# Optimization experiments

Measured on AMD Instinct MI355X. Metric: run time of the kernel, lower is better.

The kernel has to match this reference:

```python
import jax, jax.numpy as jnp
import numpy as np

N_NODES = 40000
N_EDGES = 640000
D = 128
BN_EPS = 1e-5
GATE_EPS = 1e-6


def _linear_params(key, d_in, d_out):
    kw, kb = jax.random.split(key)
    bound = 1.0 / np.sqrt(d_in)
    W = jax.random.uniform(kw, (d_out, d_in), jnp.float32, -bound, bound)
    b = jax.random.uniform(kb, (d_out,), jnp.float32, -bound, bound)
    return W, b


def setup_inputs() -> dict:
    key = jax.random.key(0)
    ks = jax.random.split(key, 8)
    x = jax.random.normal(ks[0], (N_NODES, D), jnp.float32)
    edge_index = jax.random.randint(ks[1], (2, N_EDGES), 0, N_NODES, jnp.int64)
    edge_attr = jax.random.normal(ks[2], (N_EDGES, D), jnp.float32)
    W_src_gate, b_src_gate = _linear_params(ks[3], D, D)
    W_dst_gate, b_dst_gate = _linear_params(ks[4], D, D)
    W_edge_gate, b_edge_gate = _linear_params(ks[5], D, D)
    W_src_update, b_src_update = _linear_params(ks[6], D, D)
    W_dst_update, b_dst_update = _linear_params(ks[7], D, D)
    return dict(
        x=x, edge_index=edge_index, edge_attr=edge_attr,
        W_src_gate=W_src_gate, b_src_gate=b_src_gate,
        W_dst_gate=W_dst_gate, b_dst_gate=b_dst_gate,
        W_edge_gate=W_edge_gate, b_edge_gate=b_edge_gate,
        W_src_update=W_src_update, b_src_update=b_src_update,
        W_dst_update=W_dst_update, b_dst_update=b_dst_update,
        bn_nodes_gamma=jnp.ones((D,), jnp.float32), bn_nodes_beta=jnp.zeros((D,), jnp.float32),
        bn_edges_gamma=jnp.ones((D,), jnp.float32), bn_edges_beta=jnp.zeros((D,), jnp.float32),
    )


def _batch_norm(z, gamma, beta):
    # training-mode BN: batch mean, biased variance (torch semantics)
    mean = jnp.mean(z, axis=0)
    var = jnp.mean(jnp.square(z - mean), axis=0)
    return gamma * (z - mean) * jax.lax.rsqrt(var + BN_EPS) + beta


def reference(x, edge_index, edge_attr,
              W_src_gate, b_src_gate, W_dst_gate, b_dst_gate,
              W_edge_gate, b_edge_gate, W_src_update, b_src_update,
              W_dst_update, b_dst_update,
              bn_nodes_gamma, bn_nodes_beta, bn_edges_gamma, bn_edges_beta):
    row, col = edge_index[0], edge_index[1]
    num_nodes = x.shape[0]
    x_row = x[row]                      # [E, D] gather
    x_col = x[col]                      # [E, D] gather
    e_src = x_row @ W_src_gate.T + b_src_gate
    e_dst = x_col @ W_dst_gate.T + b_dst_gate
    m = e_src + e_dst + edge_attr @ W_edge_gate.T + b_edge_gate  # [E, D]
    sigma = jax.nn.sigmoid(m)
    h_weighted = (x_col @ W_dst_update.T + b_dst_update) * sigma
    h_sum = jax.ops.segment_sum(h_weighted, col, num_segments=num_nodes)
    sigma_sum = jax.ops.segment_sum(sigma, col, num_segments=num_nodes)
    h_normalized = h_sum / (sigma_sum + GATE_EPS)
    x_new = x @ W_src_update.T + b_src_update + h_normalized
    x_new = jax.nn.softplus(_batch_norm(x_new, bn_nodes_gamma, bn_nodes_beta))
    y_new = jax.nn.softplus(_batch_norm(m, bn_edges_gamma, bn_edges_beta))
    x_new = x + x_new          # residual
    y_new = edge_attr + y_new  # residual
    return (x_new, y_new)
```

## Files before the change

kernel.cpp:

```cpp
#include <hip/hip_runtime.h>

#define NN 40000
#define NE 640000

typedef unsigned short u16;
typedef unsigned int u32;
typedef __attribute__((ext_vector_type(4))) float f32x4;
typedef __attribute__((ext_vector_type(4))) float fv4;
typedef __attribute__((ext_vector_type(4))) u32 uv4;
typedef __attribute__((ext_vector_type(8))) __bf16 bf16x8;

#define LSTR 132
#define TPW 8

__device__ __forceinline__ float bf2f(u16 u) { return __uint_as_float(((u32)u) << 16); }
__device__ __forceinline__ u16 f2bf(float f) {
  u32 u = __float_as_uint(f);
  u32 r = 0x7fffu + ((u >> 16) & 1u);
  return (u16)((u + r) >> 16);
}
__device__ __forceinline__ float splus(float v) {
  return fmaxf(v, 0.0f) + __logf(1.0f + __expf(-fabsf(v)));
}

__global__ void sniff_k(const u32* __restrict__ gamma, const u32* __restrict__ eidx,
                        u32* __restrict__ flags) {
  if (threadIdx.x == 0) {
    flags[0] = (gamma[0] == 0x3F803F80u) ? 1u : 0u;
    u32 odd = eidx[1] | eidx[3] | eidx[5] | eidx[7] |
              eidx[9] | eidx[11] | eidx[13] | eidx[15];
    flags[1] = (odd == 0u) ? 1u : 0u;
  }
}

__device__ __forceinline__ int load_col(const void* eidx, int e, u32 i64) {
  int nc = i64 ? (int)((const u32*)eidx)[2 * ((size_t)NE + e)]
               : ((const int*)eidx)[NE + e];
  return min(max(nc, 0), NN - 1);
}
__device__ __forceinline__ int load_row(const void* eidx, int e, u32 i64) {
  int nr = i64 ? (int)((const u32*)eidx)[2 * (size_t)e]
               : ((const int*)eidx)[e];
  return min(max(nr, 0), NN - 1);
}

__global__ __launch_bounds__(256) void wconv5_k(
    const float* __restrict__ W0, const float* __restrict__ W1,
    const float* __restrict__ W2, const float* __restrict__ W3,
    const float* __restrict__ W4, u16* __restrict__ out) {
  int i = blockIdx.x * 256 + threadIdx.x;
  int mtx = blockIdx.y;
  const float* W = (mtx == 0) ? W0 : (mtx == 1) ? W1 : (mtx == 2) ? W2
                 : (mtx == 3) ? W3 : W4;
  out[mtx * 16384 + i] = f2bf(W[i]);
}

__global__ __launch_bounds__(256) void hist_k(const void* __restrict__ eidx,
                                              u32* __restrict__ cnt,
                                              const u32* __restrict__ flags) {
  int e = blockIdx.x * 256 + threadIdx.x;
  atomicAdd(&cnt[load_col(eidx, e, flags[1])], 1u);
}

__device__ __forceinline__ bf16x8 a_frag(const float* __restrict__ row, int kbase) {
  float4 f0 = *(const float4*)(row + kbase);
  float4 f1 = *(const float4*)(row + kbase + 4);
  bf16x8 a;
  a[0] = (__bf16)f0.x; a[1] = (__bf16)f0.y; a[2] = (__bf16)f0.z; a[3] = (__bf16)f0.w;
  a[4] = (__bf16)f1.x; a[5] = (__bf16)f1.y; a[6] = (__bf16)f1.z; a[7] = (__bf16)f1.w;
  return a;
}

__device__ __forceinline__ bf16x8 cvt8v(fv4 a, fv4 b) {
  bf16x8 r;
  r[0] = (__bf16)a[0]; r[1] = (__bf16)a[1]; r[2] = (__bf16)a[2]; r[3] = (__bf16)a[3];
  r[4] = (__bf16)b[0]; r[5] = (__bf16)b[1]; r[6] = (__bf16)b[2]; r[7] = (__bf16)b[3];
  return r;
}

__device__ __forceinline__ void gemm16(const bf16x8 af[4], const u16* __restrict__ Wb,
                                       const float* __restrict__ bias, int lane,
                                       f32x4 acc[8]) {
  int l15 = lane & 15, lk = lane >> 4;
#pragma unroll
  for (int n = 0; n < 8; ++n) {
    float bv = bias[n * 16 + l15];
    acc[n] = (f32x4){bv, bv, bv, bv};
  }
#pragma unroll
  for (int n = 0; n < 8; ++n) {
    const u16* bp = Wb + (size_t)(n * 16 + l15) * 128 + lk * 8;
#pragma unroll
    for (int k = 0; k < 4; ++k) {
      bf16x8 b = *(const bf16x8*)(bp + 32 * k);
      acc[n] = __builtin_amdgcn_mfma_f32_16x16x32_bf16(af[k], b, acc[n], 0, 0, 0);
    }
  }
}

__device__ __forceinline__ void store_tile(u16* __restrict__ out, int m0, int lane,
                                           const f32x4 acc[8]) {
  int l15 = lane & 15, lk = lane >> 4;
#pragma unroll
  for (int n = 0; n < 8; ++n)
#pragma unroll
    for (int r = 0; r < 4; ++r)
      out[(size_t)(m0 + lk * 4 + r) * 128 + n * 16 + l15] = f2bf(acc[n][r]);
}

__global__ __launch_bounds__(256) void node_gemm_k(
    const float* __restrict__ x, const u16* __restrict__ Wb,
    const float* __restrict__ B0, const float* __restrict__ B1,
    const float* __restrict__ B2, const float* __restrict__ B3,
    const u32* __restrict__ cnt,
    u16* __restrict__ o0, u16* __restrict__ o1,
    u16* __restrict__ o2, u16* __restrict__ o3,
    float* __restrict__ statsg) {
  __shared__ float red[256];
  int tid = threadIdx.x, lane = tid & 63, w = tid >> 6;
  for (int i = tid; i < 256; i += 256) red[i] = 0.f;
  __syncthreads();
  int m0 = blockIdx.x * 64 + w * 16;
  int l15 = lane & 15, lk = lane >> 4;
  const float* arow = x + (size_t)(m0 + l15) * 128;
  bf16x8 af[4];
#pragma unroll
  for (int k = 0; k < 4; ++k) af[k] = a_frag(arow, 32 * k + 8 * lk);
  f32x4 acc[8], accd[8];
  gemm16(af, Wb + 0 * 16384, B0, lane, acc);  store_tile(o0, m0, lane, acc);
  gemm16(af, Wb + 1 * 16384, B1, lane, acc);  store_tile(o1, m0, lane, acc);
  gemm16(af, Wb + 2 * 16384, B2, lane, accd); store_tile(o2, m0, lane, accd);
  gemm16(af, Wb + 3 * 16384, B3, lane, acc);  store_tile(o3, m0, lane, acc);
  float g[4];
#pragma unroll
  for (int r = 0; r < 4; ++r) g[r] = (cnt[m0 + lk * 4 + r] != 0u) ? 1.0f : 0.0f;
#pragma unroll
  for (int n = 0; n < 8; ++n) {
    float a1 = 0.f, a2 = 0.f;
#pragma unroll
    for (int r = 0; r < 4; ++r) {
      float zv = acc[n][r] + g[r] * accd[n][r];
      a1 += zv;
      a2 = fmaf(zv, zv, a2);
    }
    a1 += __shfl_xor(a1, 16); a1 += __shfl_xor(a1, 32);
    a2 += __shfl_xor(a2, 16); a2 += __shfl_xor(a2, 32);
    if (lk == 0) {
      atomicAdd(&red[n * 16 + l15], a1);
      atomicAdd(&red[128 + n * 16 + l15], a2);
    }
  }
  __syncthreads();
  for (int i = tid; i < 256; i += 256) atomicAdd(&statsg[256 + i], red[i]);
}

__global__ __launch_bounds__(256, 2) void edge_gemm_k(
    const float* __restrict__ ea, const u16* __restrict__ Wgb,
    const float* __restrict__ Bg,
    const u16* __restrict__ g_src, const u16* __restrict__ g_dst,
    const void* __restrict__ eidx,
    u16* __restrict__ mge, float* __restrict__ statsg,
    const u32* __restrict__ flags) {
  __shared__ __align__(16) char gbuf[4][16 * LSTR * 4];
  __shared__ __align__(16) u16 Wl[16384];
  int tid = threadIdx.x, lane = tid & 63, w = tid >> 6;
  int l15 = lane & 15, lk = lane >> 4;
  int el = lane >> 2, c4 = lane & 3;
  u32 i64 = flags[1];

  {
    const u32* Wg32 = (const u32*)Wgb;
    u32* Wl32 = (u32*)Wl;
#pragma unroll
    for (int j = 0; j < 32; ++j) {
      int i2 = tid + 256 * j;
      int r = i2 >> 6, c2 = i2 & 63;
      int g = c2 >> 2, win = c2 & 3;
      Wl32[r * 64 + (((g ^ ((r & 7) << 1)) << 2) | win)] = Wg32[i2];
    }
  }
  __syncthreads();

  float* gt = (float*)gbuf[w];
  u16*   mt = (u16*)gbuf[w];
  int sw = (l15 & 7) << 1;

  float bias[8];
#pragma unroll
  for (int n = 0; n < 8; ++n) bias[n] = Bg[n * 16 + l15];

  float e1[8] = {0.f, 0.f, 0.f, 0.f, 0.f, 0.f, 0.f, 0.f};
  float e2[8] = {0.f, 0.f, 0.f, 0.f, 0.f, 0.f, 0.f, 0.f};

  int base = (blockIdx.x * 4 + w) * (TPW * 16);
  const float* aptr = ea + (size_t)(base + l15) * 128 + 8 * lk;

  fv4 tmp[8];
#pragma unroll
  for (int k = 0; k < 4; ++k) {
    tmp[2 * k]     = *(const fv4*)(aptr + 32 * k);
    tmp[2 * k + 1] = *(const fv4*)(aptr + 32 * k + 4);
  }
  bf16x8 af[4];
#pragma unroll
  for (int k = 0; k < 4; ++k) af[k] = cvt8v(tmp[2 * k], tmp[2 * k + 1]);

  for (int t = 0; t < TPW; ++t) {
    int e0 = base + t * 16;
    int eg = e0 + el;
    int grow = load_row(eidx, eg, i64);
    int gcol = load_col(eidx, eg, i64);
#pragma unroll
    for (int it = 0; it < 4; ++it) {
      uv4 gsv = *(const uv4*)(g_src + (size_t)grow * 128 + c4 * 8 + it * 32);
      uv4 gdv = *(const uv4*)(g_dst + (size_t)gcol * 128 + c4 * 8 + it * 32);
      const u16* sp = (const u16*)&gsv;
      const u16* dp = (const u16*)&gdv;
      fv4 lo, hi;
#pragma unroll
      for (int j = 0; j < 4; ++j) lo[j] = bf2f(sp[j]) + bf2f(dp[j]);
#pragma unroll
      for (int j = 0; j < 4; ++j) hi[j] = bf2f(sp[4 + j]) + bf2f(dp[4 + j]);
      int ch = c4 + 4 * it;
      *(fv4*)(gt + el * LSTR + ch * 8)     = lo;
      *(fv4*)(gt + el * LSTR + ch * 8 + 4) = hi;
    }
    if (t + 1 < TPW) {
      const float* anx = aptr + (size_t)(t + 1) * 16 * 128;
#pragma unroll
      for (int k = 0; k < 4; ++k) {
        tmp[2 * k]     = *(const fv4*)(anx + 32 * k);
        tmp[2 * k + 1] = *(const fv4*)(anx + 32 * k + 4);
      }
    }
    f32x4 acc[8];
#pragma unroll
    for (int n = 0; n < 8; ++n)
      acc[n] = (f32x4){bias[n], bias[n], bias[n], bias[n]};
#pragma unroll
    for (int n = 0; n < 8; ++n)
#pragma unroll
      for (int k = 0; k < 4; ++k) {
        bf16x8 b = *(const bf16x8*)(Wl + ((n * 16 + l15) << 7) +
                                    (((lk + 4 * k) ^ sw) << 3));
        acc[n] = __builtin_amdgcn_mfma_f32_16x16x32_bf16(af[k], b, acc[n], 0, 0, 0);
      }
    float g32[8][4];
#pragma unroll
    for (int n = 0; n < 8; ++n)
#pragma unroll
      for (int r = 0; r < 4; ++r)
        g32[n][r] = gt[(lk * 4 + r) * LSTR + n * 16 + l15];
    __builtin_amdgcn_sched_barrier(0);
#pragma unroll
    for (int n = 0; n < 8; ++n)
#pragma unroll
      for (int r = 0; r < 4; ++r) {
        float mv = acc[n][r] + g32[n][r];
        e1[n] += mv;
        e2[n] = fmaf(mv, mv, e2[n]);
        mt[(lk * 4 + r) * LSTR + n * 16 + l15] = f2bf(mv);
      }
    if (t + 1 < TPW) {
#pragma unroll
      for (int k = 0; k < 4; ++k) af[k] = cvt8v(tmp[2 * k], tmp[2 * k + 1]);
    }
#pragma unroll
    for (int it = 0; it < 4; ++it) {
      int ch = c4 + 4 * it;
      uint4 v = *(const uint4*)(mt + el * LSTR + ch * 8);
      *(uint4*)(mge + (size_t)(e0 + el) * 128 + ch * 8) = v;
    }
  }
#pragma unroll
  for (int n = 0; n < 8; ++n) {
    float s1 = e1[n], s2 = e2[n];
    s1 += __shfl_xor(s1, 16); s1 += __shfl_xor(s1, 32);
    s2 += __shfl_xor(s2, 16); s2 += __shfl_xor(s2, 32);
    if (lk == 0) {
      atomicAdd(&statsg[n * 16 + l15], s1);
      atomicAdd(&statsg[128 + n * 16 + l15], s2);
    }
  }
}

__global__ void stats_fin_k(const float* __restrict__ es1, const float* __restrict__ es2,
                            const float* __restrict__ ns1, const float* __restrict__ ns2,
                            const float* __restrict__ eg_, const float* __restrict__ eb_,
                            const float* __restrict__ ng_, const float* __restrict__ nb_,
                            float* __restrict__ params) {
  int d = threadIdx.x;
  float em = es1[d] * (1.0f / NE);
  float ev = fmaxf(es2[d] * (1.0f / NE) - em * em, 0.0f);
  float esc = eg_[d] * rsqrtf(ev + 1e-5f);
  params[d] = esc;
  params[128 + d] = eb_[d] - em * esc;
  float nm = ns1[d] * (1.0f / NN);
  float nv = fmaxf(ns2[d] * (1.0f / NN) - nm * nm, 0.0f);
  float nsc = ng_[d] * rsqrtf(nv + 1e-5f);
  params[256 + d] = nsc;
  params[384 + d] = nb_[d] - nm * nsc;
}

__global__ __launch_bounds__(256) void node_fin2_k(
    const float* __restrict__ x, const u16* __restrict__ us,
    const u16* __restrict__ ud, const u32* __restrict__ cnt,
    const float* __restrict__ params, float* __restrict__ out) {
  size_t t = (size_t)blockIdx.x * 256 + threadIdx.x;
  size_t base = t * 8;
  int d0 = (int)(base & 127);
  int n = (int)(t >> 4);
  float g = (cnt[n] != 0u) ? 1.0f : 0.0f;
  float4 xa = *(const float4*)(x + base);
  float4 xb = *(const float4*)(x + base + 4);
  float xv[8] = {xa.x, xa.y, xa.z, xa.w, xb.x, xb.y, xb.z, xb.w};
  uint4 usv = *(const uint4*)(us + base);
  uint4 udv = *(const uint4*)(ud + base);
  const u16* up = (const u16*)&usv;
  const u16* dp = (const u16*)&udv;
  float o[8];
#pragma unroll
  for (int j = 0; j < 8; ++j) {
    float z = bf2f(up[j]) + g * bf2f(dp[j]);
    float bnv = z * params[256 + d0 + j] + params[384 + d0 + j];
    o[j] = xv[j] + splus(bnv);
  }
  *(float4*)(out + base) = make_float4(o[0], o[1], o[2], o[3]);
  *(float4*)(out + base + 4) = make_float4(o[4], o[5], o[6], o[7]);
}

__global__ __launch_bounds__(256) void edge_fin_k(
    const float* __restrict__ edge_attr, const u16* __restrict__ mge,
    const float* __restrict__ params, float* __restrict__ out) {
  size_t t = (size_t)blockIdx.x * 256 + threadIdx.x;
  size_t base = t * 8;
  int d0 = (int)(base & 127);
  float4 ea = *(const float4*)(edge_attr + base);
  float4 eb = *(const float4*)(edge_attr + base + 4);
  float ev[8] = {ea.x, ea.y, ea.z, ea.w, eb.x, eb.y, eb.z, eb.w};
  uint4 mv_ = *(const uint4*)(mge + base);
  const u16* mp = (const u16*)&mv_;
  float o[8];
#pragma unroll
  for (int j = 0; j < 8; ++j) {
    float m = bf2f(mp[j]);
    float bnv = m * params[d0 + j] + params[128 + d0 + j];
    o[j] = ev[j] + splus(bnv);
  }
  *(float4*)(out + base) = make_float4(o[0], o[1], o[2], o[3]);
  *(float4*)(out + base + 4) = make_float4(o[4], o[5], o[6], o[7]);
}

extern "C" void kernel_launch(void* const* d_in, const int* in_sizes, int n_in,
                              void* d_out, int out_size, void* d_ws, size_t ws_size,
                              hipStream_t stream) {
  const float* x        = (const float*)d_in[0];
  const void*  eidx     = d_in[1];
  const float* edge_att = (const float*)d_in[2];
  const float* Wsg = (const float*)d_in[3];  const float* bsg = (const float*)d_in[4];
  const float* Wdg = (const float*)d_in[5];  const float* bdg = (const float*)d_in[6];
  const float* Weg = (const float*)d_in[7];  const float* beg = (const float*)d_in[8];
  const float* Wsu = (const float*)d_in[9];  const float* bsu = (const float*)d_in[10];
  const float* Wdu = (const float*)d_in[11]; const float* bdu = (const float*)d_in[12];
  const float* bng = (const float*)d_in[13]; const float* bnb = (const float*)d_in[14];
  const float* beg_g = (const float*)d_in[15]; const float* beb = (const float*)d_in[16];

  char* ws = (char*)d_ws;
  u16*   g_src  = (u16*)(ws + 0);
  u16*   g_dst  = (u16*)(ws + 10240000);
  u16*   u_dst  = (u16*)(ws + 20480000);
  u16*   u_src  = (u16*)(ws + 30720000);
  float* stats  = (float*)(ws + 40960000);
  u32*   flags  = (u32*)(ws + 40964096);
  u16*   wbuf   = (u16*)(ws + 40968192);
  u32*   cnt    = (u32*)(ws + 41132032);
  u16*   mge    = (u16*)(ws + 41292032);

  hipMemsetAsync(stats, 0, 4096, stream);
  hipMemsetAsync(cnt, 0, 160000, stream);

  sniff_k<<<1, 64, 0, stream>>>((const u32*)bng, (const u32*)eidx, flags);
  wconv5_k<<<dim3(64, 5), 256, 0, stream>>>(Wsg, Wdg, Wdu, Wsu, Weg, wbuf);
  hist_k<<<NE / 256, 256, 0, stream>>>(eidx, cnt, flags);
  node_gemm_k<<<NN / 64, 256, 0, stream>>>(x, wbuf, bsg, bdg, bdu, bsu, cnt,
                                           g_src, g_dst, u_dst, u_src, stats);
  edge_gemm_k<<<NE / (64 * TPW), 256, 0, stream>>>(edge_att, wbuf + 4 * 16384, beg,
                                                   g_src, g_dst, eidx,
                                                   mge, stats, flags);
  stats_fin_k<<<1, 128, 0, stream>>>(stats, stats + 128, stats + 256, stats + 384,
                                     beg_g, beb, bng, bnb, stats + 512);
  node_fin2_k<<<(NN * 128) / 2048, 256, 0, stream>>>(x, u_src, u_dst, cnt,
                                                     stats + 512, (float*)d_out);
  edge_fin_k<<<(NE * 128) / 2048, 256, 0, stream>>>(edge_att, mge, stats + 512,
                                                    (float*)d_out + (size_t)NN * 128);
}
```

Before: 473.0 us.

## Software-pipeline gathered node-gate rows and edge indices across edge tiles

The edge-gate kernel now prefetches the gathered g_src/g_dst rows for the next 16-edge tile into double-buffered registers, and the edge indices two tiles ahead, while the current tile's MFMAs run. It also fully unrolls the tile loop and moves the bf16 add/LDS staging after the MFMAs. The aim is to hide the latency of the random gathers, which were previously issued and consumed right away. In exchange it uses more VGPRs, which may lower occupancy.

```diff
diff --git a/kernel.cpp b/kernel.cpp
--- a/kernel.cpp
+++ b/kernel.cpp
@@ -195,36 +195,30 @@
   int base = (blockIdx.x * 4 + w) * (TPW * 16);
   const float* aptr = ea + (size_t)(base + l15) * 128 + 8 * lk;
 
+  int rowc = load_row(eidx, base + el, i64);
+  int colc = load_col(eidx, base + el, i64);
   fv4 tmp[8];
 #pragma unroll
   for (int k = 0; k < 4; ++k) {
     tmp[2 * k]     = *(const fv4*)(aptr + 32 * k);
     tmp[2 * k + 1] = *(const fv4*)(aptr + 32 * k + 4);
   }
+  uv4 gsv[2][4], gdv[2][4];
+#pragma unroll
+  for (int it = 0; it < 4; ++it) {
+    gsv[0][it] = *(const uv4*)(g_src + (size_t)rowc * 128 + c4 * 8 + it * 32);
+    gdv[0][it] = *(const uv4*)(g_dst + (size_t)colc * 128 + c4 * 8 + it * 32);
+  }
+  int rown = load_row(eidx, base + 16 + el, i64);
+  int coln = load_col(eidx, base + 16 + el, i64);
   bf16x8 af[4];
 #pragma unroll
   for (int k = 0; k < 4; ++k) af[k] = cvt8v(tmp[2 * k], tmp[2 * k + 1]);
 
+#pragma unroll
   for (int t = 0; t < TPW; ++t) {
+    int cur = t & 1, nxt = cur ^ 1;
     int e0 = base + t * 16;
-    int eg = e0 + el;
-    int grow = load_row(eidx, eg, i64);
-    int gcol = load_col(eidx, eg, i64);
-#pragma unroll
-    for (int it = 0; it < 4; ++it) {
-      uv4 gsv = *(const uv4*)(g_src + (size_t)grow * 128 + c4 * 8 + it * 32);
-      uv4 gdv = *(const uv4*)(g_dst + (size_t)gcol * 128 + c4 * 8 + it * 32);
-      const u16* sp = (const u16*)&gsv;
-      const u16* dp = (const u16*)&gdv;
-      fv4 lo, hi;
-#pragma unroll
-      for (int j = 0; j < 4; ++j) lo[j] = bf2f(sp[j]) + bf2f(dp[j]);
-#pragma unroll
-      for (int j = 0; j < 4; ++j) hi[j] = bf2f(sp[4 + j]) + bf2f(dp[4 + j]);
-      int ch = c4 + 4 * it;
-      *(fv4*)(gt + el * LSTR + ch * 8)     = lo;
-      *(fv4*)(gt + el * LSTR + ch * 8 + 4) = hi;
-    }
     if (t + 1 < TPW) {
       const float* anx = aptr + (size_t)(t + 1) * 16 * 128;
 #pragma unroll
@@ -232,6 +226,18 @@
         tmp[2 * k]     = *(const fv4*)(anx + 32 * k);
         tmp[2 * k + 1] = *(const fv4*)(anx + 32 * k + 4);
       }
+    }
+    if (t + 1 < TPW) {
+#pragma unroll
+      for (int it = 0; it < 4; ++it) {
+        gsv[nxt][it] = *(const uv4*)(g_src + (size_t)rown * 128 + c4 * 8 + it * 32);
+        gdv[nxt][it] = *(const uv4*)(g_dst + (size_t)coln * 128 + c4 * 8 + it * 32);
+      }
+    }
+    int rn2 = rown, cn2 = coln;
+    if (t + 2 < TPW) {
+      rn2 = load_row(eidx, base + (t + 2) * 16 + el, i64);
+      cn2 = load_col(eidx, base + (t + 2) * 16 + el, i64);
     }
     f32x4 acc[8];
 #pragma unroll
@@ -245,6 +251,19 @@
                                     (((lk + 4 * k) ^ sw) << 3));
         acc[n] = __builtin_amdgcn_mfma_f32_16x16x32_bf16(af[k], b, acc[n], 0, 0, 0);
       }
+#pragma unroll
+    for (int it = 0; it < 4; ++it) {
+      const u16* sp = (const u16*)&gsv[cur][it];
+      const u16* dp = (const u16*)&gdv[cur][it];
+      fv4 lo, hi;
+#pragma unroll
+      for (int j = 0; j < 4; ++j) lo[j] = bf2f(sp[j]) + bf2f(dp[j]);
+#pragma unroll
+      for (int j = 0; j < 4; ++j) hi[j] = bf2f(sp[4 + j]) + bf2f(dp[4 + j]);
+      int ch = c4 + 4 * it;
+      *(fv4*)(gt + el * LSTR + ch * 8)     = lo;
+      *(fv4*)(gt + el * LSTR + ch * 8 + 4) = hi;
+    }
     float g32[8][4];
 #pragma unroll
     for (int n = 0; n < 8; ++n)
@@ -261,16 +280,17 @@
         e2[n] = fmaf(mv, mv, e2[n]);
         mt[(lk * 4 + r) * LSTR + n * 16 + l15] = f2bf(mv);
       }
-    if (t + 1 < TPW) {
-#pragma unroll
-      for (int k = 0; k < 4; ++k) af[k] = cvt8v(tmp[2 * k], tmp[2 * k + 1]);
-    }
 #pragma unroll
     for (int it = 0; it < 4; ++it) {
       int ch = c4 + 4 * it;
       uint4 v = *(const uint4*)(mt + el * LSTR + ch * 8);
       *(uint4*)(mge + (size_t)(e0 + el) * 128 + ch * 8) = v;
     }
+    if (t + 1 < TPW) {
+#pragma unroll
+      for (int k = 0; k < 4; ++k) af[k] = cvt8v(tmp[2 * k], tmp[2 * k + 1]);
+    }
+    rown = rn2; coln = cn2;
   }
 #pragma unroll
   for (int n = 0; n < 8; ++n) {
```

Result: slower. 554.1 us (+17.1%).

## Split edge gather into separate kernel writing pre-summed bf16 to mge

Applied to the files above, without the earlier changes.

Adds a gather_k kernel that loads the src/dst gate projections for each edge, sums them, and writes the bf16 result into the mge buffer. edge_gemm_k then reads this contiguous buffer, prefetched one tile ahead, instead of doing indirect gathers inside the MFMA loop. The aim is to take random-access latency out of the GEMM kernel. In exchange it adds an extra kernel launch, a full E×128 bf16 write and read-back, and an extra bf16 rounding of the sum.

```diff
diff --git a/kernel.cpp b/kernel.cpp
--- a/kernel.cpp
+++ b/kernel.cpp
@@ -60,6 +60,34 @@
                                               const u32* __restrict__ flags) {
   int e = blockIdx.x * 256 + threadIdx.x;
   atomicAdd(&cnt[load_col(eidx, e, flags[1])], 1u);
+}
+
+__global__ __launch_bounds__(256) void gather_k(
+    const void* __restrict__ eidx,
+    const u16* __restrict__ g_src, const u16* __restrict__ g_dst,
+    u16* __restrict__ mge, const u32* __restrict__ flags) {
+  int tid = threadIdx.x;
+  u32 i64 = flags[1];
+  int es = tid >> 4;
+  int d0 = (tid & 15) * 8;
+  int base = blockIdx.x * 256;
+  for (int k = 0; k < 16; ++k) {
+    int e = base + k * 16 + es;
+    int row = load_row(eidx, e, i64);
+    int col = load_col(eidx, e, i64);
+    uint4 sv = *(const uint4*)(g_src + (size_t)row * 128 + d0);
+    uint4 dv = *(const uint4*)(g_dst + (size_t)col * 128 + d0);
+    const u16* sp = (const u16*)&sv;
+    const u16* dp = (const u16*)&dv;
+    u32 pk[4];
+#pragma unroll
+    for (int j = 0; j < 4; ++j) {
+      u16 a = f2bf(bf2f(sp[2 * j]) + bf2f(dp[2 * j]));
+      u16 b = f2bf(bf2f(sp[2 * j + 1]) + bf2f(dp[2 * j + 1]));
+      pk[j] = (u32)a | ((u32)b << 16);
+    }
+    *(uint4*)(mge + (size_t)e * 128 + d0) = make_uint4(pk[0], pk[1], pk[2], pk[3]);
+  }
 }
 
 __device__ __forceinline__ bf16x8 a_frag(const float* __restrict__ row, int kbase) {
@@ -157,16 +185,12 @@
 __global__ __launch_bounds__(256, 2) void edge_gemm_k(
     const float* __restrict__ ea, const u16* __restrict__ Wgb,
     const float* __restrict__ Bg,
-    const u16* __restrict__ g_src, const u16* __restrict__ g_dst,
-    const void* __restrict__ eidx,
-    u16* __restrict__ mge, float* __restrict__ statsg,
-    const u32* __restrict__ flags) {
+    u16* __restrict__ mge, float* __restrict__ statsg) {
   __shared__ __align__(16) char gbuf[4][16 * LSTR * 4];
   __shared__ __align__(16) u16 Wl[16384];
   int tid = threadIdx.x, lane = tid & 63, w = tid >> 6;
   int l15 = lane & 15, lk = lane >> 4;
   int el = lane >> 2, c4 = lane & 3;
-  u32 i64 = flags[1];
 
   {
     const u32* Wg32 = (const u32*)Wgb;
@@ -201,26 +225,24 @@
     tmp[2 * k]     = *(const fv4*)(aptr + 32 * k);
     tmp[2 * k + 1] = *(const fv4*)(aptr + 32 * k + 4);
   }
+  uv4 muv[4];
+#pragma unroll
+  for (int it = 0; it < 4; ++it)
+    muv[it] = *(const uv4*)(mge + (size_t)(base + el) * 128 + c4 * 8 + it * 32);
   bf16x8 af[4];
 #pragma unroll
   for (int k = 0; k < 4; ++k) af[k] = cvt8v(tmp[2 * k], tmp[2 * k + 1]);
 
   for (int t = 0; t < TPW; ++t) {
     int e0 = base + t * 16;
-    int eg = e0 + el;
-    int grow = load_row(eidx, eg, i64);
-    int gcol = load_col(eidx, eg, i64);
 #pragma unroll
     for (int it = 0; it < 4; ++it) {
-      uv4 gsv = *(const uv4*)(g_src + (size_t)grow * 128 + c4 * 8 + it * 32);
-      uv4 gdv = *(const uv4*)(g_dst + (size_t)gcol * 128 + c4 * 8 + it * 32);
-      const u16* sp = (const u16*)&gsv;
-      const u16* dp = (const u16*)&gdv;
+      const u16* mp = (const u16*)&muv[it];
       fv4 lo, hi;
 #pragma unroll
-      for (int j = 0; j < 4; ++j) lo[j] = bf2f(sp[j]) + bf2f(dp[j]);
-#pragma unroll
-      for (int j = 0; j < 4; ++j) hi[j] = bf2f(sp[4 + j]) + bf2f(dp[4 + j]);
+      for (int j = 0; j < 4; ++j) lo[j] = bf2f(mp[j]);
+#pragma unroll
+      for (int j = 0; j < 4; ++j) hi[j] = bf2f(mp[4 + j]);
       int ch = c4 + 4 * it;
       *(fv4*)(gt + el * LSTR + ch * 8)     = lo;
       *(fv4*)(gt + el * LSTR + ch * 8 + 4) = hi;
@@ -232,6 +254,11 @@
         tmp[2 * k]     = *(const fv4*)(anx + 32 * k);
         tmp[2 * k + 1] = *(const fv4*)(anx + 32 * k + 4);
       }
+    }
+    if (t + 1 < TPW) {
+#pragma unroll
+      for (int it = 0; it < 4; ++it)
+        muv[it] = *(const uv4*)(mge + (size_t)(e0 + 16 + el) * 128 + c4 * 8 + it * 32);
     }
     f32x4 acc[8];
 #pragma unroll
@@ -384,9 +411,9 @@
   hist_k<<<NE / 256, 256, 0, stream>>>(eidx, cnt, flags);
   node_gemm_k<<<NN / 64, 256, 0, stream>>>(x, wbuf, bsg, bdg, bdu, bsu, cnt,
                                            g_src, g_dst, u_dst, u_src, stats);
+  gather_k<<<NE / 256, 256, 0, stream>>>(eidx, g_src, g_dst, mge, flags);
   edge_gemm_k<<<NE / (64 * TPW), 256, 0, stream>>>(edge_att, wbuf + 4 * 16384, beg,
-                                                   g_src, g_dst, eidx,
-                                                   mge, stats, flags);
+                                                   mge, stats);
   stats_fin_k<<<1, 128, 0, stream>>>(stats, stats + 128, stats + 256, stats + 384,
                                      beg_g, beb, bng, bnb, stats + 512);
   node_fin2_k<<<(NN * 128) / 2048, 256, 0, stream>>>(x, u_src, u_dst, cnt,
```

Result: slower. 520.4 us (+10.0%).
